# Optimization experiments

Hardware: AMD Instinct MI355X
Metric: run time of the kernel (lower is better)

Reference implementation:

```python
import jax, jax.numpy as jnp
import numpy as np

B, D, H, W = 8, 768, 32, 32
C, K = 2, 8
COORD_DIM = 128
GRID = 16
DIST_THRESH = 5
NUM_STEPS = 3
STEP_SIZE = 0.1
HW = H * W


def _pair_indices():
    # Static grid of sampled points (stride = max(1, H//grid_size)) and all
    # ordered pairs with Manhattan distance in (0, 5] -- mirrors the torch loops.
    stride = max(1, H // GRID)
    pi, pj = np.meshgrid(np.arange(0, H, stride), np.arange(0, W, stride), indexing='ij')
    pi, pj = pi.ravel(), pj.ravel()
    d = np.abs(pi[:, None] - pi[None, :]) + np.abs(pj[:, None] - pj[None, :])
    a, b = np.nonzero((d > 0) & (d <= DIST_THRESH))
    return (pi[a] * W + pj[a]).astype(np.int32), (pi[b] * W + pj[b]).astype(np.int32)


def setup_inputs() -> dict:
    key = jax.random.key(0)
    ks = jax.random.split(key, 16)
    IN = 2 * D + COORD_DIM  # 1664

    def n(i, shape, s=1.0):
        return jax.random.normal(ks[i], shape, dtype=jnp.float32) * s

    return {
        'features': n(0, (B, D, H, W)),
        'cam_raw': jax.random.uniform(ks[1], (B, C, H, W), dtype=jnp.float32),
        'y_primary': jax.random.uniform(ks[2], (B, C), dtype=jnp.float32),
        'eps': n(3, (B, K)),
        'coord_emb': n(4, (256 * 256, COORD_DIM), 0.02),
        'aff_W1': n(5, (C, IN, 256), 0.02), 'aff_b1': jnp.zeros((C, 256), jnp.float32),
        'aff_W2': n(6, (C, 256, 128), 0.05), 'aff_b2': jnp.zeros((C, 128), jnp.float32),
        'aff_W3': n(7, (C, 128, 1), 0.05), 'aff_b3': jnp.zeros((C, 1), jnp.float32),
        'mu_W1': n(8, (D, 256), 0.02), 'mu_b1': jnp.zeros((256,), jnp.float32),
        'mu_W2': n(9, (256, K), 0.05), 'mu_b2': jnp.zeros((K,), jnp.float32),
        'ls_W1': n(10, (D, 256), 0.02), 'ls_b1': jnp.zeros((256,), jnp.float32),
        'ls_W2': n(11, (256, K), 0.05), 'ls_b2': jnp.zeros((K,), jnp.float32),
        'conf_scale': jnp.array(1.0, jnp.float32),
        'conf_bias': jnp.array(0.0, jnp.float32),
    }


def reference(features, cam_raw, y_primary, eps, coord_emb,
              aff_W1, aff_b1, aff_W2, aff_b2, aff_W3, aff_b3,
              mu_W1, mu_b1, mu_W2, mu_b2, ls_W1, ls_b1, ls_W2, ls_b2,
              conf_scale, conf_bias):
    idx_a_np, idx_b_np = _pair_indices()
    idx_a, idx_b = jnp.asarray(idx_a_np), jnp.asarray(idx_b_np)
    P = idx_a.shape[0]

    # --- SubClassPosterior on globally pooled features ---
    f_global = features.mean(axis=(2, 3))                      # (B, D)
    z_mu = jax.nn.relu(f_global @ mu_W1 + mu_b1) @ mu_W2 + mu_b2
    z_logstd = jax.nn.relu(f_global @ ls_W1 + ls_b1) @ ls_W2 + ls_b2
    z_samples = z_mu + jnp.exp(z_logstd) * eps

    # --- ClassConditionalAffinity: batched gather + grouped MLP over all pairs ---
    feat = features.reshape(B, D, HW)
    f1 = feat[:, :, idx_a].transpose(0, 2, 1)                  # (B, P, D)
    f2 = feat[:, :, idx_b].transpose(0, 2, 1)                  # (B, P, D)
    ce = 0.5 * (coord_emb[idx_a] + coord_emb[idx_b])           # (P, E)
    x = jnp.concatenate([f1, f2, jnp.broadcast_to(ce, (B, P, COORD_DIM))], axis=-1)
    h = jax.nn.relu(jnp.einsum('bpi,cio->bcpo', x, aff_W1) + aff_b1[:, None, :])
    h = jax.nn.relu(jnp.einsum('bcpi,cio->bcpo', h, aff_W2) + aff_b2[:, None, :])
    logit = (jnp.einsum('bcpi,cio->bcpo', h, aff_W3) + aff_b3[:, None, :])[..., 0]
    val = jax.nn.sigmoid(logit)                                # (B, C, P)

    # A = where(mask, sigmoid(mlp), I); pairs are strictly off-diagonal & unique
    A = jnp.broadcast_to(jnp.eye(HW, dtype=features.dtype), (B, C, HW, HW))
    A = A.at[:, :, idx_a, idx_b].set(val)
    A = A / (A.sum(axis=3, keepdims=True) + 1e-8)              # row-normalize

    # --- AnisotropicDiffusion: M <- M + dt * (A M - deg * M) ---
    M = cam_raw.reshape(B, C, HW)
    deg = A.sum(axis=3)                                        # (B, C, HW)
    for _ in range(NUM_STEPS):
        L = jnp.einsum('bcij,bcj->bci', A, M) - deg * M
        M = M + STEP_SIZE * L
    cam_refined = jnp.clip(M.reshape(B, C, H, W), 0.0, 1.0)

    confidence = jax.nn.sigmoid(conf_scale * cam_refined + conf_bias)
    return cam_refined, z_mu, z_logstd, z_samples, A, confidence
```

## Files before the change

### kernel.cpp

```cpp
#include <hip/hip_runtime.h>
#include <math.h>

#define BB 8
#define DD 768
#define HWN 1024
#define NS 256
#define PPAD 3072
#define O1 256
#define O2 128

typedef __attribute__((ext_vector_type(8))) short bf16x8;
typedef __attribute__((ext_vector_type(4))) float f32x4;

__constant__ int c_du[12] = {1,-1,0,0,2,-2,0,0,1, 1,-1,-1};
__constant__ int c_dv[12] = {0, 0,1,-1,0, 0,2,-2,1,-1, 1,-1};
__constant__ signed char c_rk[25] = {
  -1,-1, 5,-1,-1,
  -1,11, 1,10,-1,
   7, 3,-1, 2, 6,
  -1, 9, 0, 8,-1,
  -1,-1, 4,-1,-1};

__device__ inline ushort f2bf(float x) {
  unsigned u = __float_as_uint(x);
  u += 0x7FFF + ((u >> 16) & 1);
  return (ushort)(u >> 16);
}
__device__ inline float bf2f(ushort h) { return __uint_as_float(((unsigned)h) << 16); }

__global__ void __launch_bounds__(256) k_pre(const float* __restrict__ feat,
    const float* __restrict__ cemb, const float* __restrict__ W1,
    const float* __restrict__ b1, const float* __restrict__ W2,
    float* __restrict__ fg, ushort* __restrict__ g16,
    float* __restrict__ EH, ushort* __restrict__ WT16, ushort* __restrict__ W2T16) {
  __shared__ __align__(16) float sm[64 * 65];
  int blk = blockIdx.x;
  int t = threadIdx.x;
  if (blk < 6144) {
    int row = blk;
    const float4 v = reinterpret_cast<const float4*>(feat + (size_t)row * HWN)[t];
    float s = v.x + v.y + v.z + v.w;
#pragma unroll
    for (int m = 32; m >= 1; m >>= 1) s += __shfl_xor(s, m, 64);
    if ((t & 63) == 0) sm[t >> 6] = s;
    if ((t & 8) == 0) {
      int b = row / DD, d = row - b * DD;
      int u = t >> 4, r = t & 7;
      int s1 = u * 16 + 2 * r;
      g16[((size_t)(b * NS + s1)) * DD + d] = f2bf(v.x);
      g16[((size_t)(b * NS + s1 + 1)) * DD + d] = f2bf(v.z);
    }
    __syncthreads();
    if (t == 0) fg[row] = (sm[0] + sm[1] + sm[2] + sm[3]) * (1.0f / 1024.0f);
  } else if (blk < 6656) {
    int bs = blk - 6144;
    int c = bs >> 8, s = bs & 255;
    int u = s >> 4, v = s & 15;
    int pix = (u << 6) + (v << 1);
    float* ce = sm;
    if (t < 128) ce[t] = cemb[(size_t)pix * 128 + t];
    __syncthreads();
    const float* W = W1 + ((size_t)c * 1664 + 1536) * O1;
    float acc = 0.f;
    for (int e = 0; e < 128; e++) acc = fmaf(ce[e], W[(size_t)e * O1 + t], acc);
    EH[((size_t)(c * NS + s)) * O1 + t] = 0.5f * (acc + b1[c * O1 + t]);
  } else {
    int r0 = blk - 6656;
    const float* src; ushort* dst; int K, N, k0, n0;
    if (r0 < 192) {
      int ch = r0 / 48, r = r0 % 48;
      int c = ch & 1, half = ch >> 1;
      src = W1 + ((size_t)c * 1664 + half * 768) * 256;
      dst = WT16 + (size_t)ch * 256 * 768;
      K = 768; N = 256; k0 = (r >> 2) * 64; n0 = (r & 3) * 64;
    } else {
      int r = r0 - 192;
      int c = r >> 3; int q = r & 7;
      src = W2 + (size_t)c * 256 * 128;
      dst = W2T16 + (size_t)c * 128 * 256;
      K = 256; N = 128; k0 = (q >> 1) * 64; n0 = (q & 1) * 64;
    }
    float (*T)[65] = reinterpret_cast<float(*)[65]>(sm);
    for (int i = 0; i < 16; i++) {
      int idx = i * 256 + t; int kl = idx >> 6, nl = idx & 63;
      T[kl][nl] = src[(size_t)(k0 + kl) * N + n0 + nl];
    }
    __syncthreads();
    for (int i = 0; i < 16; i++) {
      int idx = i * 256 + t; int nl = idx >> 6, kl = idx & 63;
      dst[(size_t)(n0 + nl) * K + k0 + kl] = f2bf(T[kl][nl]);
    }
  }
}

__global__ void __launch_bounds__(256) k_mid(const ushort* __restrict__ g16,
    const ushort* __restrict__ WT16, const float* __restrict__ EHb,
    const float* __restrict__ fg, const float* __restrict__ muW1,
    const float* __restrict__ lsW1,
    ushort* __restrict__ Fb16, float* __restrict__ zscr) {
  __shared__ __align__(16) float sm[4096];
  int blk = blockIdx.x;
  int t = threadIdx.x;
  if (blk < 512) {
    int mt = blk & 31, nt = (blk >> 5) & 3, ch = blk >> 7;
    int c = ch & 1;
    int row0 = mt * 64, col0 = nt * 64;
    int wid = t >> 6, l = t & 63;
    int wm = wid & 1, wn = wid >> 1;
    int lm = l & 15, lk = (l >> 4) * 8;
    float (*ehs)[64] = reinterpret_cast<float(*)[64]>(sm);
    int s0 = row0 & 255;
    for (int i = 0; i < 16; i++) {
      int idx = i * 256 + t; int rl = idx >> 6, nl = idx & 63;
      ehs[rl][nl] = EHb[((size_t)(c * 256 + s0 + rl)) * 256 + col0 + nl];
    }
    f32x4 acc[2][2] = {};
    const ushort* ap0 = g16 + (size_t)(row0 + wm * 32 + lm) * DD + lk;
    const ushort* bp0 = WT16 + ((size_t)ch * 256 + col0 + wn * 32 + lm) * DD + lk;
#pragma unroll 4
    for (int k0 = 0; k0 < DD; k0 += 32) {
      bf16x8 a0 = *(const bf16x8*)(ap0 + k0);
      bf16x8 a1 = *(const bf16x8*)(ap0 + 16 * DD + k0);
      bf16x8 b0 = *(const bf16x8*)(bp0 + k0);
      bf16x8 b1 = *(const bf16x8*)(bp0 + 16 * DD + k0);
      acc[0][0] = __builtin_amdgcn_mfma_f32_16x16x32_bf16(a0, b0, acc[0][0], 0, 0, 0);
      acc[0][1] = __builtin_amdgcn_mfma_f32_16x16x32_bf16(a0, b1, acc[0][1], 0, 0, 0);
      acc[1][0] = __builtin_amdgcn_mfma_f32_16x16x32_bf16(a1, b0, acc[1][0], 0, 0, 0);
      acc[1][1] = __builtin_amdgcn_mfma_f32_16x16x32_bf16(a1, b1, acc[1][1], 0, 0, 0);
    }
    __syncthreads();
#pragma unroll
    for (int i = 0; i < 2; i++)
#pragma unroll
      for (int jj = 0; jj < 2; jj++)
#pragma unroll
        for (int r = 0; r < 4; r++) {
          int rm = wm * 32 + i * 16 + (l >> 4) * 4 + r;
          int cn = wn * 32 + jj * 16 + lm;
          float vo = acc[i][jj][r] + ehs[rm][cn];
          Fb16[((size_t)ch * 2048 + row0 + rm) * 256 + col0 + cn] = f2bf(vo);
        }
  } else {
    int i = blk - 512;
    int chunk = i % 6, path = (i / 6) & 1, b = i / 12;
    int rg = t >> 6, ct = t & 63;
    float* sf = sm;
    float (*red)[256] = reinterpret_cast<float(*)[256]>(sm + 128);
    if (t < 128) sf[t] = fg[b * DD + chunk * 128 + t];
    __syncthreads();
    const float* W = (path ? lsW1 : muW1) + (size_t)(chunk * 128) * 256;
    float acc[4] = {0.f, 0.f, 0.f, 0.f};
#pragma unroll 4
    for (int it = 0; it < 32; it++) {
      int d = it * 4 + rg;
      float f = sf[d];
      float4 w = *reinterpret_cast<const float4*>(W + (size_t)d * 256 + ct * 4);
      acc[0] = fmaf(f, w.x, acc[0]);
      acc[1] = fmaf(f, w.y, acc[1]);
      acc[2] = fmaf(f, w.z, acc[2]);
      acc[3] = fmaf(f, w.w, acc[3]);
    }
    *reinterpret_cast<float4*>(&red[rg][ct * 4]) =
        make_float4(acc[0], acc[1], acc[2], acc[3]);
    __syncthreads();
    zscr[(((size_t)(b * 2 + path)) * 6 + chunk) * 256 + t] =
        red[0][t] + red[1][t] + red[2][t] + red[3][t];
  }
}

__global__ void __launch_bounds__(256) k_pair(const ushort* __restrict__ Fb16,
    const ushort* __restrict__ W2T16, const float* __restrict__ b2,
    const float* __restrict__ W3, const float* __restrict__ b3,
    const float* __restrict__ zscr,
    const float* __restrict__ mub1, const float* __restrict__ muW2,
    const float* __restrict__ mub2,
    const float* __restrict__ lsb1, const float* __restrict__ lsW2,
    const float* __restrict__ lsb2, const float* __restrict__ eps,
    float* __restrict__ val,
    float* __restrict__ o_zmu, float* __restrict__ o_zls, float* __restrict__ o_zs) {
  __shared__ __align__(16) ushort h1s[64 * 256];
  __shared__ float psum2[2][64];
  int blk = blockIdx.x;
  int t = threadIdx.x;
  if (blk < 768) {
    int bc = blk / 48, grp = blk - bc * 48;
    int b = bc >> 1, c = bc & 1;
    int wid = t >> 6, l = t & 63;
    int wm = wid & 1, wn = wid >> 1;
    int lm = l & 15, lk = (l >> 4) * 8;
    {
      int p_l = t >> 2, q = t & 3;
      int j = grp * 64 + p_l;
      int s = j / 12, ko = j - s * 12;
      int u = s >> 4, v = s & 15;
      int ub = u + c_du[ko], vb = v + c_dv[ko];
      bool vld = (ub >= 0) && (ub < 16) && (vb >= 0) && (vb < 16);
      int sb = vld ? ub * 16 + vb : s;
      const ushort* f1p = Fb16 + ((size_t)(c * 2048 + b * 256 + s)) * 256 + q * 64;
      const ushort* f2p = Fb16 + ((size_t)((2 + c) * 2048 + b * 256 + sb)) * 256 + q * 64;
      char* hb = (char*)h1s;
#pragma unroll
      for (int kk = 0; kk < 64; kk += 8) {
        bf16x8 x1 = *(const bf16x8*)(f1p + kk);
        bf16x8 x2 = *(const bf16x8*)(f2p + kk);
        bf16x8 o;
#pragma unroll
        for (int e = 0; e < 8; e++) {
          float a = bf2f((ushort)x1[e]) + bf2f((ushort)x2[e]);
          o[e] = (short)f2bf(fmaxf(a, 0.f));
        }
        int byt = (p_l * 512 + (q * 64 + kk) * 2) ^ ((p_l & 7) << 4);
        *(bf16x8*)(hb + byt) = o;
      }
    }
    __syncthreads();
    f32x4 acc[2][4] = {};
    const ushort* wp = W2T16 + ((size_t)(c * 128 + wn * 64 + lm)) * 256 + lk;
    const char* hb = (const char*)h1s;
    int p0 = wm * 32 + lm;
    int swz = (p0 & 7) << 4;
#pragma unroll 2
    for (int k0 = 0; k0 < 256; k0 += 32) {
      bf16x8 a0 = *(const bf16x8*)(hb + ((p0 * 512 + (k0 + lk) * 2) ^ swz));
      bf16x8 a1 = *(const bf16x8*)(hb + (((p0 + 16) * 512 + (k0 + lk) * 2) ^ swz));
#pragma unroll
      for (int nf = 0; nf < 4; nf++) {
        bf16x8 bb = *(const bf16x8*)(wp + nf * 16 * 256 + k0);
        acc[0][nf] = __builtin_amdgcn_mfma_f32_16x16x32_bf16(a0, bb, acc[0][nf], 0, 0, 0);
        acc[1][nf] = __builtin_amdgcn_mfma_f32_16x16x32_bf16(a1, bb, acc[1][nf], 0, 0, 0);
      }
    }
    float b2v[4], w3v[4];
#pragma unroll
    for (int nf = 0; nf < 4; nf++) {
      int col = wn * 64 + nf * 16 + lm;
      b2v[nf] = b2[c * 128 + col];
      w3v[nf] = W3[c * 128 + col];
    }
    float part[2][4];
#pragma unroll
    for (int mf = 0; mf < 2; mf++)
#pragma unroll
      for (int r = 0; r < 4; r++) {
        float ssum = 0.f;
#pragma unroll
        for (int nf = 0; nf < 4; nf++) {
          float h = fmaxf(acc[mf][nf][r] + b2v[nf], 0.f);
          ssum = fmaf(h, w3v[nf], ssum);
        }
        part[mf][r] = ssum;
      }
#pragma unroll
    for (int m = 1; m <= 8; m <<= 1)
#pragma unroll
      for (int mf = 0; mf < 2; mf++)
#pragma unroll
        for (int r = 0; r < 4; r++)
          part[mf][r] += __shfl_xor(part[mf][r], m, 64);
    if (lm == 0) {
#pragma unroll
      for (int mf = 0; mf < 2; mf++)
#pragma unroll
        for (int r = 0; r < 4; r++)
          psum2[wn][wm * 32 + mf * 16 + (l >> 4) * 4 + r] = part[mf][r];
    }
    __syncthreads();
    if (t < 64) {
      int jj = grp * 64 + t;
      int ss = jj / 12, kk2 = jj - ss * 12;
      int uu = ss >> 4, vv2 = ss & 15;
      int ub2 = uu + c_du[kk2], vb2 = vv2 + c_dv[kk2];
      bool vld = (ub2 >= 0) && (ub2 < 16) && (vb2 >= 0) && (vb2 < 16);
      float lg = psum2[0][t] + psum2[1][t] + b3[c];
      float sv = 1.0f / (1.0f + expf(-lg));
      val[(size_t)bc * PPAD + jj] = vld ? sv : 0.0f;
    }
  } else {
    int b = blk - 768;
    float* shm = (float*)h1s;
    float* shl = shm + 256;
    float* zres = shm + 512;
    float hm = mub1[t], hl = lsb1[t];
#pragma unroll
    for (int ch = 0; ch < 6; ch++) {
      hm += zscr[(((size_t)(b * 2 + 0)) * 6 + ch) * 256 + t];
      hl += zscr[(((size_t)(b * 2 + 1)) * 6 + ch) * 256 + t];
    }
    shm[t] = fmaxf(hm, 0.f);
    shl[t] = fmaxf(hl, 0.f);
    __syncthreads();
    if (t < 128 && (t & 63) < 8) {
      int path = t >> 6, kk = t & 7;
      const float* W2p = path ? lsW2 : muW2;
      const float* bi = path ? lsb2 : mub2;
      const float* sh = path ? shl : shm;
      float z = bi[kk];
      for (int i = 0; i < 256; i++) z = fmaf(sh[i], W2p[i * 8 + kk], z);
      zres[path * 8 + kk] = z;
    }
    __syncthreads();
    if (t < 8) {
      float zm = zres[t], zl = zres[8 + t];
      o_zmu[b * 8 + t] = zm;
      o_zls[b * 8 + t] = zl;
      o_zs[b * 8 + t] = zm + expf(zl) * eps[b * 8 + t];
    }
  }
}

__global__ void __launch_bounds__(256) k_final(const float* __restrict__ val,
    const float* __restrict__ cam,
    const float* __restrict__ csc, const float* __restrict__ cbi,
    float* __restrict__ A, float* __restrict__ o_cam, float* __restrict__ o_conf) {
  __shared__ float smf[260];
  int blk = blockIdx.x;
  int t = threadIdx.x;
  if (blk < 16384) {
    int bc = blk >> 10, row = blk & 1023;
    size_t base = (size_t)bc * HWN * HWN + (size_t)row * HWN;
    int pi = row >> 5, pj = row & 31;
    float4 o = make_float4(0.f, 0.f, 0.f, 0.f);
    if (((pi | pj) & 1) == 0) {
      int u = pi >> 1, v = pj >> 1;
      int s = u * 16 + v;
      float* sv = smf;
      if (t < 12) sv[t] = val[(size_t)bc * PPAD + s * 12 + t];
      __syncthreads();
      if (t == 0) {
        float ssum = 1.f;
        for (int k = 0; k < 12; k++) ssum += sv[k];
        smf[12] = 1.f / (ssum + 1e-8f);
      }
      __syncthreads();
      float inv = smf[12];
      float vo[4];
#pragma unroll
      for (int e = 0; e < 4; e++) {
        int col = t * 4 + e;
        float x = 0.f;
        if (col == row) {
          x = inv;
        } else if ((col & 33) == 0) {
          int cu = col >> 6, cv = (col & 31) >> 1;
          int du = cu - u + 2, dv = cv - v + 2;
          if (((unsigned)du < 5u) && ((unsigned)dv < 5u)) {
            int k = c_rk[du * 5 + dv];
            if (k >= 0) x = sv[k] * inv;
          }
        }
        vo[e] = x;
      }
      o = make_float4(vo[0], vo[1], vo[2], vo[3]);
    } else {
      if ((row >> 2) == t) {
        float dv = 1.0f / (1.0f + 1e-8f);
        int e = row & 3;
        if (e == 0) o.x = dv; else if (e == 1) o.y = dv;
        else if (e == 2) o.z = dv; else o.w = dv;
      }
    }
    reinterpret_cast<float4*>(A + base)[t] = o;
  } else {
    int bc = blk - 16384;
    float* M = smf;
    int u = t >> 4, v = t & 15;
    int pix = (u << 6) + (v << 1);
    const float* camr = cam + (size_t)bc * HWN;
    float m = camr[pix];
    float vv[12];
    int nb[12];
    float ssum = 1.f;
#pragma unroll
    for (int k = 0; k < 12; k++) {
      int ub = u + c_du[k], vb = v + c_dv[k];
      bool vld = (ub >= 0) && (ub < 16) && (vb >= 0) && (vb < 16);
      nb[k] = vld ? ub * 16 + vb : t;
      vv[k] = vld ? val[(size_t)bc * PPAD + t * 12 + k] : 0.0f;
      ssum += vv[k];
    }
    float inv = 1.0f / (ssum + 1e-8f);
    float degn = ssum * inv;
    M[t] = m;
    __syncthreads();
    for (int step = 0; step < 3; step++) {
      float accv = m;
#pragma unroll
      for (int k = 0; k < 12; k++) accv = fmaf(vv[k], M[nb[k]], accv);
      float L = accv * inv - degn * m;
      m = fmaf(0.1f, L, m);
      __syncthreads();
      M[t] = m;
      __syncthreads();
    }
    float scale = csc[0], bias = cbi[0];
    for (int p = t; p < HWN; p += 256) {
      int ppi = p >> 5, ppj = p & 31;
      float x;
      if (((ppi | ppj) & 1) == 0) x = M[(ppi >> 1) * 16 + (ppj >> 1)];
      else x = camr[p];
      x = fminf(fmaxf(x, 0.0f), 1.0f);
      o_cam[(size_t)bc * HWN + p] = x;
      o_conf[(size_t)bc * HWN + p] = 1.0f / (1.0f + expf(-(scale * x + bias)));
    }
  }
}

extern "C" void kernel_launch(void* const* d_in, const int* in_sizes, int n_in,
                              void* d_out, int out_size, void* d_ws, size_t ws_size,
                              hipStream_t stream) {
  const float* feat = (const float*)d_in[0];
  const float* cam  = (const float*)d_in[1];
  const float* eps  = (const float*)d_in[3];
  const float* cemb = (const float*)d_in[4];
  const float* aW1  = (const float*)d_in[5];
  const float* ab1  = (const float*)d_in[6];
  const float* aW2  = (const float*)d_in[7];
  const float* ab2  = (const float*)d_in[8];
  const float* aW3  = (const float*)d_in[9];
  const float* ab3  = (const float*)d_in[10];
  const float* muW1 = (const float*)d_in[11];
  const float* mub1 = (const float*)d_in[12];
  const float* muW2 = (const float*)d_in[13];
  const float* mub2 = (const float*)d_in[14];
  const float* lsW1 = (const float*)d_in[15];
  const float* lsb1 = (const float*)d_in[16];
  const float* lsW2 = (const float*)d_in[17];
  const float* lsb2 = (const float*)d_in[18];
  const float* csc  = (const float*)d_in[19];
  const float* cbi  = (const float*)d_in[20];

  float* out = (float*)d_out;
  float* o_cam  = out;
  float* o_zmu  = out + 16384;
  float* o_zls  = out + 16448;
  float* o_zs   = out + 16512;
  float* o_A    = out + 16576;
  float* o_conf = out + 16793792;

  float*  fg    = o_A;
  float*  EHb   = o_A + 6144;
  ushort* g16   = (ushort*)(o_A + 137216);
  ushort* WT16  = (ushort*)(o_A + 923648);
  ushort* W2T16 = (ushort*)(o_A + 1316864);
  ushort* Fb16  = (ushort*)(o_A + 1349632);
  float*  zscr  = o_A + 2398208;
  float*  valb  = (float*)d_ws;

  hipLaunchKernelGGL(k_pre, dim3(6864), dim3(256), 0, stream,
                     feat, cemb, aW1, ab1, aW2, fg, g16, EHb, WT16, W2T16);
  hipLaunchKernelGGL(k_mid, dim3(608), dim3(256), 0, stream,
                     g16, WT16, EHb, fg, muW1, lsW1, Fb16, zscr);
  hipLaunchKernelGGL(k_pair, dim3(776), dim3(256), 0, stream,
                     Fb16, W2T16, ab2, aW3, ab3, zscr,
                     mub1, muW2, mub2, lsb1, lsW2, lsb2, eps,
                     valb, o_zmu, o_zls, o_zs);
  hipLaunchKernelGGL(k_final, dim3(16400), dim3(256), 0, stream,
                     valb, cam, csc, cbi, o_A, o_cam, o_conf);
}
```

Baseline: 85.08 us.

## Spread identity-row writes of A across earlier kernels to overlap with compute

After: 83.90 us, median of 2. About the same (-1.4%).

```diff
diff --git a/kernel.cpp b/kernel.cpp
--- a/kernel.cpp
+++ b/kernel.cpp
@@ -8,6 +8,8 @@
 #define PPAD 3072
 #define O1 256
 #define O2 128
+#define SCRATCH_ROWS 2366
+#define FILL_SPLIT 7009
 
 typedef __attribute__((ext_vector_type(8))) short bf16x8;
 typedef __attribute__((ext_vector_type(4))) float f32x4;
@@ -27,6 +29,21 @@
   return (ushort)(u >> 16);
 }
 __device__ inline float bf2f(ushort h) { return __uint_as_float(((unsigned)h) << 16); }
+
+__device__ inline void identity_row(float* __restrict__ A, int r_g, int t) {
+  int row = r_g & 1023;
+  float4 o = make_float4(0.f, 0.f, 0.f, 0.f);
+  if ((row >> 2) == t) {
+    float dv = 1.0f / (1.0f + 1e-8f);
+    int e = row & 3;
+    if (e == 0) o.x = dv; else if (e == 1) o.y = dv;
+    else if (e == 2) o.z = dv; else o.w = dv;
+  }
+  reinterpret_cast<float4*>(A + (size_t)r_g * 1024)[t] = o;
+}
+__device__ inline bool row_sampled(int row) {
+  return ((row | (row >> 5)) & 1) == 0;
+}
 
 __global__ void __launch_bounds__(256) k_pre(const float* __restrict__ feat,
     const float* __restrict__ cemb, const float* __restrict__ W1,
@@ -97,10 +114,15 @@
     const ushort* __restrict__ WT16, const float* __restrict__ EHb,
     const float* __restrict__ fg, const float* __restrict__ muW1,
     const float* __restrict__ lsW1,
-    ushort* __restrict__ Fb16, float* __restrict__ zscr) {
+    ushort* __restrict__ Fb16, float* __restrict__ zscr, float* __restrict__ A) {
   __shared__ __align__(16) float sm[4096];
   int blk = blockIdx.x;
   int t = threadIdx.x;
+  if (blk >= 608) {
+    int r_g = SCRATCH_ROWS + (blk - 608);
+    if (!row_sampled(r_g & 1023)) identity_row(A, r_g, t);
+    return;
+  }
   if (blk < 512) {
     int mt = blk & 31, nt = (blk >> 5) & 3, ch = blk >> 7;
     int c = ch & 1;
@@ -177,11 +199,17 @@
     const float* __restrict__ lsb1, const float* __restrict__ lsW2,
     const float* __restrict__ lsb2, const float* __restrict__ eps,
     float* __restrict__ val,
-    float* __restrict__ o_zmu, float* __restrict__ o_zls, float* __restrict__ o_zs) {
+    float* __restrict__ o_zmu, float* __restrict__ o_zls, float* __restrict__ o_zs,
+    float* __restrict__ A) {
   __shared__ __align__(16) ushort h1s[64 * 256];
   __shared__ float psum2[2][64];
   int blk = blockIdx.x;
   int t = threadIdx.x;
+  if (blk >= 776) {
+    int r_g = SCRATCH_ROWS + FILL_SPLIT + (blk - 776);
+    if (!row_sampled(r_g & 1023)) identity_row(A, r_g, t);
+    return;
+  }
   if (blk < 768) {
     int bc = blk / 48, grp = blk - bc * 48;
     int b = bc >> 1, c = bc & 1;
@@ -315,53 +343,45 @@
   __shared__ float smf[260];
   int blk = blockIdx.x;
   int t = threadIdx.x;
-  if (blk < 16384) {
-    int bc = blk >> 10, row = blk & 1023;
+  if (blk < 4096) {
+    int bc = blk >> 8, s = blk & 255;
+    int u = s >> 4, v = s & 15;
+    int row = u * 64 + 2 * v;
     size_t base = (size_t)bc * HWN * HWN + (size_t)row * HWN;
-    int pi = row >> 5, pj = row & 31;
-    float4 o = make_float4(0.f, 0.f, 0.f, 0.f);
-    if (((pi | pj) & 1) == 0) {
-      int u = pi >> 1, v = pj >> 1;
-      int s = u * 16 + v;
-      float* sv = smf;
-      if (t < 12) sv[t] = val[(size_t)bc * PPAD + s * 12 + t];
-      __syncthreads();
-      if (t == 0) {
-        float ssum = 1.f;
-        for (int k = 0; k < 12; k++) ssum += sv[k];
-        smf[12] = 1.f / (ssum + 1e-8f);
+    float* sv = smf;
+    if (t < 12) sv[t] = val[(size_t)bc * PPAD + s * 12 + t];
+    __syncthreads();
+    if (t == 0) {
+      float ssum = 1.f;
+      for (int k = 0; k < 12; k++) ssum += sv[k];
+      smf[12] = 1.f / (ssum + 1e-8f);
+    }
+    __syncthreads();
+    float inv = smf[12];
+    float vo[4];
+#pragma unroll
+    for (int e = 0; e < 4; e++) {
+      int col = t * 4 + e;
+      float x = 0.f;
+      if (col == row) {
+        x = inv;
+      } else if ((col & 33) == 0) {
+        int cu = col >> 6, cv = (col & 31) >> 1;
+        int du = cu - u + 2, dv = cv - v + 2;
+        if (((unsigned)du < 5u) && ((unsigned)dv < 5u)) {
+          int k = c_rk[du * 5 + dv];
+          if (k >= 0) x = sv[k] * inv;
+        }
       }
-      __syncthreads();
-      float inv = smf[12];
-      float vo[4];
-#pragma unroll
-      for (int e = 0; e < 4; e++) {
-        int col = t * 4 + e;
-        float x = 0.f;
-        if (col == row) {
-          x = inv;
-        } else if ((col & 33) == 0) {
-          int cu = col >> 6, cv = (col & 31) >> 1;
-          int du = cu - u + 2, dv = cv - v + 2;
-          if (((unsigned)du < 5u) && ((unsigned)dv < 5u)) {
-            int k = c_rk[du * 5 + dv];
-            if (k >= 0) x = sv[k] * inv;
-          }
-        }
-        vo[e] = x;
-      }
-      o = make_float4(vo[0], vo[1], vo[2], vo[3]);
-    } else {
-      if ((row >> 2) == t) {
-        float dv = 1.0f / (1.0f + 1e-8f);
-        int e = row & 3;
-        if (e == 0) o.x = dv; else if (e == 1) o.y = dv;
-        else if (e == 2) o.z = dv; else o.w = dv;
-      }
-    }
-    reinterpret_cast<float4*>(A + base)[t] = o;
+      vo[e] = x;
+    }
+    reinterpret_cast<float4*>(A + base)[t] =
+        make_float4(vo[0], vo[1], vo[2], vo[3]);
+  } else if (blk < 4096 + SCRATCH_ROWS) {
+    int r_g = blk - 4096;
+    if (!row_sampled(r_g & 1023)) identity_row(A, r_g, t);
   } else {
-    int bc = blk - 16384;
+    int bc = blk - (4096 + SCRATCH_ROWS);
     float* M = smf;
     int u = t >> 4, v = t & 15;
     int pix = (u << 6) + (v << 1);
@@ -448,12 +468,13 @@
 
   hipLaunchKernelGGL(k_pre, dim3(6864), dim3(256), 0, stream,
                      feat, cemb, aW1, ab1, aW2, fg, g16, EHb, WT16, W2T16);
-  hipLaunchKernelGGL(k_mid, dim3(608), dim3(256), 0, stream,
-                     g16, WT16, EHb, fg, muW1, lsW1, Fb16, zscr);
-  hipLaunchKernelGGL(k_pair, dim3(776), dim3(256), 0, stream,
+  hipLaunchKernelGGL(k_mid, dim3(608 + FILL_SPLIT), dim3(256), 0, stream,
+                     g16, WT16, EHb, fg, muW1, lsW1, Fb16, zscr, o_A);
+  hipLaunchKernelGGL(k_pair, dim3(776 + (16384 - SCRATCH_ROWS - FILL_SPLIT)),
+                     dim3(256), 0, stream,
                      Fb16, W2T16, ab2, aW3, ab3, zscr,
                      mub1, muW2, mub2, lsb1, lsW2, lsb2, eps,
-                     valb, o_zmu, o_zls, o_zs);
-  hipLaunchKernelGGL(k_final, dim3(16400), dim3(256), 0, stream,
+                     valb, o_zmu, o_zls, o_zs, o_A);
+  hipLaunchKernelGGL(k_final, dim3(4096 + SCRATCH_ROWS + 16), dim3(256), 0, stream,
                      valb, cam, csc, cbi, o_A, o_cam, o_conf);
 }
```

## Distribute dense A writes into earlier kernels and shrink final diffusion kernel

Applied to the files above, without the earlier changes.

Measured after the change: 84.15 us. No clear change (-1.1%).

```diff
diff --git a/kernel.cpp b/kernel.cpp
--- a/kernel.cpp
+++ b/kernel.cpp
@@ -28,11 +28,16 @@
 }
 __device__ inline float bf2f(ushort h) { return __uint_as_float(((unsigned)h) << 16); }
 
-__global__ void __launch_bounds__(256) k_pre(const float* __restrict__ feat,
+__device__ inline bool row_sampled(int row) {
+  return ((row | (row >> 5)) & 1) == 0;
+}
+
+__global__ void __launch_bounds__(256) k1(const float* __restrict__ feat,
     const float* __restrict__ cemb, const float* __restrict__ W1,
     const float* __restrict__ b1, const float* __restrict__ W2,
     float* __restrict__ fg, ushort* __restrict__ g16,
-    float* __restrict__ EH, ushort* __restrict__ WT16, ushort* __restrict__ W2T16) {
+    float* __restrict__ EH, ushort* __restrict__ WT16, ushort* __restrict__ W2T16,
+    float* __restrict__ A) {
   __shared__ __align__(16) float sm[64 * 65];
   int blk = blockIdx.x;
   int t = threadIdx.x;
@@ -64,7 +69,7 @@
     float acc = 0.f;
     for (int e = 0; e < 128; e++) acc = fmaf(ce[e], W[(size_t)e * O1 + t], acc);
     EH[((size_t)(c * NS + s)) * O1 + t] = 0.5f * (acc + b1[c * O1 + t]);
-  } else {
+  } else if (blk < 6864) {
     int r0 = blk - 6656;
     const float* src; ushort* dst; int K, N, k0, n0;
     if (r0 < 192) {
@@ -90,10 +95,27 @@
       int idx = i * 256 + t; int nl = idx >> 6, kl = idx & 63;
       dst[(size_t)(n0 + nl) * K + k0 + kl] = f2bf(T[kl][nl]);
     }
-  }
-}
-
-__global__ void __launch_bounds__(256) k_mid(const ushort* __restrict__ g16,
+  } else {
+    int r0 = (blk - 6864) * 8;
+#pragma unroll
+    for (int i = 0; i < 8; i++) {
+      int r_g = r0 + i;
+      int row = r_g & 1023;
+      if (!row_sampled(row)) {
+        float4 o = make_float4(0.f, 0.f, 0.f, 0.f);
+        if ((row >> 2) == t) {
+          float dv = 1.0f / (1.0f + 1e-8f);
+          int e = row & 3;
+          if (e == 0) o.x = dv; else if (e == 1) o.y = dv;
+          else if (e == 2) o.z = dv; else o.w = dv;
+        }
+        reinterpret_cast<float4*>(A + (size_t)r_g * 1024)[t] = o;
+      }
+    }
+  }
+}
+
+__global__ void __launch_bounds__(256) k2(const ushort* __restrict__ g16,
     const ushort* __restrict__ WT16, const float* __restrict__ EHb,
     const float* __restrict__ fg, const float* __restrict__ muW1,
     const float* __restrict__ lsW1,
@@ -168,7 +190,7 @@
   }
 }
 
-__global__ void __launch_bounds__(256) k_pair(const ushort* __restrict__ Fb16,
+__global__ void __launch_bounds__(256) k3(const ushort* __restrict__ Fb16,
     const ushort* __restrict__ W2T16, const float* __restrict__ b2,
     const float* __restrict__ W3, const float* __restrict__ b3,
     const float* __restrict__ zscr,
@@ -177,24 +199,31 @@
     const float* __restrict__ lsb1, const float* __restrict__ lsW2,
     const float* __restrict__ lsb2, const float* __restrict__ eps,
     float* __restrict__ val,
-    float* __restrict__ o_zmu, float* __restrict__ o_zls, float* __restrict__ o_zs) {
+    float* __restrict__ o_zmu, float* __restrict__ o_zls, float* __restrict__ o_zs,
+    float* __restrict__ A) {
   __shared__ __align__(16) ushort h1s[64 * 256];
   __shared__ float psum2[2][64];
+  __shared__ float sval[64];
+  __shared__ float sinv[8];
   int blk = blockIdx.x;
   int t = threadIdx.x;
-  if (blk < 768) {
-    int bc = blk / 48, grp = blk - bc * 48;
+  if (blk < 832) {
+    int bc = blk / 52, grp = blk - bc * 52;
     int b = bc >> 1, c = bc & 1;
+    int site0 = grp * 5;
+    int nsit = (site0 + 5 <= 256) ? 5 : (256 - site0);
+    int npairs = nsit * 12;
     int wid = t >> 6, l = t & 63;
     int wm = wid & 1, wn = wid >> 1;
     int lm = l & 15, lk = (l >> 4) * 8;
     {
       int p_l = t >> 2, q = t & 3;
-      int j = grp * 64 + p_l;
-      int s = j / 12, ko = j - s * 12;
+      int sl = p_l / 12, ko = p_l - sl * 12;
+      bool realp = p_l < npairs;
+      int s = site0 + (realp ? sl : 0);
       int u = s >> 4, v = s & 15;
       int ub = u + c_du[ko], vb = v + c_dv[ko];
-      bool vld = (ub >= 0) && (ub < 16) && (vb >= 0) && (vb < 16);
+      bool vld = realp && (ub >= 0) && (ub < 16) && (vb >= 0) && (vb < 16);
       int sb = vld ? ub * 16 + vb : s;
       const ushort* f1p = Fb16 + ((size_t)(c * 2048 + b * 256 + s)) * 256 + q * 64;
       const ushort* f2p = Fb16 + ((size_t)((2 + c) * 2048 + b * 256 + sb)) * 256 + q * 64;
@@ -266,17 +295,55 @@
     }
     __syncthreads();
     if (t < 64) {
-      int jj = grp * 64 + t;
-      int ss = jj / 12, kk2 = jj - ss * 12;
+      int pl = t;
+      int sl2 = pl / 12, ko2 = pl - sl2 * 12;
+      bool realp2 = pl < npairs;
+      int ss = site0 + (realp2 ? sl2 : 0);
       int uu = ss >> 4, vv2 = ss & 15;
-      int ub2 = uu + c_du[kk2], vb2 = vv2 + c_dv[kk2];
-      bool vld = (ub2 >= 0) && (ub2 < 16) && (vb2 >= 0) && (vb2 < 16);
+      int ub2 = uu + c_du[ko2], vb2 = vv2 + c_dv[ko2];
+      bool vld2 = realp2 && (ub2 >= 0) && (ub2 < 16) && (vb2 >= 0) && (vb2 < 16);
       float lg = psum2[0][t] + psum2[1][t] + b3[c];
       float sv = 1.0f / (1.0f + expf(-lg));
-      val[(size_t)bc * PPAD + jj] = vld ? sv : 0.0f;
+      float outv = vld2 ? sv : 0.0f;
+      sval[t] = outv;
+      if (realp2) val[(size_t)bc * PPAD + site0 * 12 + pl] = outv;
+    }
+    __syncthreads();
+    if (t < nsit) {
+      float ssum = 1.f;
+#pragma unroll
+      for (int k = 0; k < 12; k++) ssum += sval[t * 12 + k];
+      sinv[t] = 1.f / (ssum + 1e-8f);
+    }
+    __syncthreads();
+    for (int sl3 = 0; sl3 < nsit; sl3++) {
+      int ss = site0 + sl3;
+      int uu = ss >> 4, vv = ss & 15;
+      int row = uu * 64 + 2 * vv;
+      size_t base = (size_t)bc * HWN * HWN + (size_t)row * HWN;
+      float inv = sinv[sl3];
+      float vo[4];
+#pragma unroll
+      for (int e = 0; e < 4; e++) {
+        int col = t * 4 + e;
+        float x = 0.f;
+        if (col == row) {
+          x = inv;
+        } else if ((col & 33) == 0) {
+          int cu = col >> 6, cv = (col & 31) >> 1;
+          int du = cu - uu + 2, dv = cv - vv + 2;
+          if (((unsigned)du < 5u) && ((unsigned)dv < 5u)) {
+            int k = c_rk[du * 5 + dv];
+            if (k >= 0) x = sval[sl3 * 12 + k] * inv;
+          }
+        }
+        vo[e] = x;
+      }
+      reinterpret_cast<float4*>(A + base)[t] =
+          make_float4(vo[0], vo[1], vo[2], vo[3]);
     }
   } else {
-    int b = blk - 768;
+    int b = blk - 832;
     float* shm = (float*)h1s;
     float* shl = shm + 256;
     float* zres = shm + 512;
@@ -308,100 +375,51 @@
   }
 }
 
-__global__ void __launch_bounds__(256) k_final(const float* __restrict__ val,
-    const float* __restrict__ cam,
+__global__ void __launch_bounds__(256) k4(const float* __restrict__ cam,
+    const float* __restrict__ val,
     const float* __restrict__ csc, const float* __restrict__ cbi,
-    float* __restrict__ A, float* __restrict__ o_cam, float* __restrict__ o_conf) {
-  __shared__ float smf[260];
-  int blk = blockIdx.x;
+    float* __restrict__ o_cam, float* __restrict__ o_conf) {
+  __shared__ float M[NS];
+  int bc = blockIdx.x;
   int t = threadIdx.x;
-  if (blk < 16384) {
-    int bc = blk >> 10, row = blk & 1023;
-    size_t base = (size_t)bc * HWN * HWN + (size_t)row * HWN;
-    int pi = row >> 5, pj = row & 31;
-    float4 o = make_float4(0.f, 0.f, 0.f, 0.f);
-    if (((pi | pj) & 1) == 0) {
-      int u = pi >> 1, v = pj >> 1;
-      int s = u * 16 + v;
-      float* sv = smf;
-      if (t < 12) sv[t] = val[(size_t)bc * PPAD + s * 12 + t];
-      __syncthreads();
-      if (t == 0) {
-        float ssum = 1.f;
-        for (int k = 0; k < 12; k++) ssum += sv[k];
-        smf[12] = 1.f / (ssum + 1e-8f);
-      }
-      __syncthreads();
-      float inv = smf[12];
-      float vo[4];
-#pragma unroll
-      for (int e = 0; e < 4; e++) {
-        int col = t * 4 + e;
-        float x = 0.f;
-        if (col == row) {
-          x = inv;
-        } else if ((col & 33) == 0) {
-          int cu = col >> 6, cv = (col & 31) >> 1;
-          int du = cu - u + 2, dv = cv - v + 2;
-          if (((unsigned)du < 5u) && ((unsigned)dv < 5u)) {
-            int k = c_rk[du * 5 + dv];
-            if (k >= 0) x = sv[k] * inv;
-          }
-        }
-        vo[e] = x;
-      }
-      o = make_float4(vo[0], vo[1], vo[2], vo[3]);
-    } else {
-      if ((row >> 2) == t) {
-        float dv = 1.0f / (1.0f + 1e-8f);
-        int e = row & 3;
-        if (e == 0) o.x = dv; else if (e == 1) o.y = dv;
-        else if (e == 2) o.z = dv; else o.w = dv;
-      }
-    }
-    reinterpret_cast<float4*>(A + base)[t] = o;
-  } else {
-    int bc = blk - 16384;
-    float* M = smf;
-    int u = t >> 4, v = t & 15;
-    int pix = (u << 6) + (v << 1);
-    const float* camr = cam + (size_t)bc * HWN;
-    float m = camr[pix];
-    float vv[12];
-    int nb[12];
-    float ssum = 1.f;
-#pragma unroll
-    for (int k = 0; k < 12; k++) {
-      int ub = u + c_du[k], vb = v + c_dv[k];
-      bool vld = (ub >= 0) && (ub < 16) && (vb >= 0) && (vb < 16);
-      nb[k] = vld ? ub * 16 + vb : t;
-      vv[k] = vld ? val[(size_t)bc * PPAD + t * 12 + k] : 0.0f;
-      ssum += vv[k];
-    }
-    float inv = 1.0f / (ssum + 1e-8f);
-    float degn = ssum * inv;
+  int u = t >> 4, v = t & 15;
+  int pix = (u << 6) + (v << 1);
+  const float* camr = cam + (size_t)bc * HWN;
+  float m = camr[pix];
+  float vv[12];
+  int nb[12];
+  float ssum = 1.f;
+#pragma unroll
+  for (int k = 0; k < 12; k++) {
+    int ub = u + c_du[k], vb = v + c_dv[k];
+    bool vld = (ub >= 0) && (ub < 16) && (vb >= 0) && (vb < 16);
+    nb[k] = vld ? ub * 16 + vb : t;
+    vv[k] = vld ? val[(size_t)bc * PPAD + t * 12 + k] : 0.0f;
+    ssum += vv[k];
+  }
+  float inv = 1.0f / (ssum + 1e-8f);
+  float degn = ssum * inv;
+  M[t] = m;
+  __syncthreads();
+  for (int step = 0; step < 3; step++) {
+    float accv = m;
+#pragma unroll
+    for (int k = 0; k < 12; k++) accv = fmaf(vv[k], M[nb[k]], accv);
+    float L = accv * inv - degn * m;
+    m = fmaf(0.1f, L, m);
+    __syncthreads();
     M[t] = m;
     __syncthreads();
-    for (int step = 0; step < 3; step++) {
-      float accv = m;
-#pragma unroll
-      for (int k = 0; k < 12; k++) accv = fmaf(vv[k], M[nb[k]], accv);
-      float L = accv * inv - degn * m;
-      m = fmaf(0.1f, L, m);
-      __syncthreads();
-      M[t] = m;
-      __syncthreads();
-    }
-    float scale = csc[0], bias = cbi[0];
-    for (int p = t; p < HWN; p += 256) {
-      int ppi = p >> 5, ppj = p & 31;
-      float x;
-      if (((ppi | ppj) & 1) == 0) x = M[(ppi >> 1) * 16 + (ppj >> 1)];
-      else x = camr[p];
-      x = fminf(fmaxf(x, 0.0f), 1.0f);
-      o_cam[(size_t)bc * HWN + p] = x;
-      o_conf[(size_t)bc * HWN + p] = 1.0f / (1.0f + expf(-(scale * x + bias)));
-    }
+  }
+  float scale = csc[0], bias = cbi[0];
+  for (int p = t; p < HWN; p += 256) {
+    int ppi = p >> 5, ppj = p & 31;
+    float x;
+    if (((ppi | ppj) & 1) == 0) x = M[(ppi >> 1) * 16 + (ppj >> 1)];
+    else x = camr[p];
+    x = fminf(fmaxf(x, 0.0f), 1.0f);
+    o_cam[(size_t)bc * HWN + p] = x;
+    o_conf[(size_t)bc * HWN + p] = 1.0f / (1.0f + expf(-(scale * x + bias)));
   }
 }
 
@@ -437,23 +455,24 @@
   float* o_A    = out + 16576;
   float* o_conf = out + 16793792;
 
-  float*  fg    = o_A;
-  float*  EHb   = o_A + 6144;
-  ushort* g16   = (ushort*)(o_A + 137216);
-  ushort* WT16  = (ushort*)(o_A + 923648);
-  ushort* W2T16 = (ushort*)(o_A + 1316864);
-  ushort* Fb16  = (ushort*)(o_A + 1349632);
-  float*  zscr  = o_A + 2398208;
-  float*  valb  = (float*)d_ws;
-
-  hipLaunchKernelGGL(k_pre, dim3(6864), dim3(256), 0, stream,
-                     feat, cemb, aW1, ab1, aW2, fg, g16, EHb, WT16, W2T16);
-  hipLaunchKernelGGL(k_mid, dim3(608), dim3(256), 0, stream,
+  float*  ws    = (float*)d_ws;
+  float*  valb  = ws;
+  float*  fg    = ws + 49152;
+  float*  EHb   = ws + 55296;
+  float*  zscr  = ws + 186368;
+  ushort* g16   = (ushort*)(ws + 210944);
+  ushort* WT16  = (ushort*)(ws + 997376);
+  ushort* W2T16 = (ushort*)(ws + 1390592);
+  ushort* Fb16  = (ushort*)(ws + 1423360);
+
+  hipLaunchKernelGGL(k1, dim3(6864 + 2048), dim3(256), 0, stream,
+                     feat, cemb, aW1, ab1, aW2, fg, g16, EHb, WT16, W2T16, o_A);
+  hipLaunchKernelGGL(k2, dim3(608), dim3(256), 0, stream,
                      g16, WT16, EHb, fg, muW1, lsW1, Fb16, zscr);
-  hipLaunchKernelGGL(k_pair, dim3(776), dim3(256), 0, stream,
+  hipLaunchKernelGGL(k3, dim3(840), dim3(256), 0, stream,
                      Fb16, W2T16, ab2, aW3, ab3, zscr,
                      mub1, muW2, mub2, lsb1, lsW2, lsb2, eps,
-                     valb, o_zmu, o_zls, o_zs);
-  hipLaunchKernelGGL(k_final, dim3(16400), dim3(256), 0, stream,
-                     valb, cam, csc, cbi, o_A, o_cam, o_conf);
-}
+                     valb, o_zmu, o_zls, o_zs, o_A);
+  hipLaunchKernelGGL(k4, dim3(16), dim3(256), 0, stream,
+                     cam, valb, csc, cbi, o_cam, o_conf);
+}
```
